# Kernel optimization log

Measured on AMD Instinct MI355X. Metric: run time of the kernel, lower is better.

## Reference

```python
import jax, jax.numpy as jnp
import numpy as np

D_MODEL = 512
NHEAD = 8
HEAD_DIM = D_MODEL // NHEAD


def setup_inputs() -> dict:
    key = jax.random.key(0)
    k1, k2, k3, k4, k5 = jax.random.split(key, 5)
    x = jax.random.normal(k1, (4, 2048, D_MODEL), dtype=jnp.float32)
    s = 1.0 / np.sqrt(D_MODEL)
    W_qkv = jax.random.normal(k2, (D_MODEL, 3 * D_MODEL), dtype=jnp.float32) * s
    b_qkv = jax.random.normal(k3, (3 * D_MODEL,), dtype=jnp.float32) * 0.01
    W_fc = jax.random.normal(k4, (D_MODEL, D_MODEL), dtype=jnp.float32) * s
    b_fc = jax.random.normal(k5, (D_MODEL,), dtype=jnp.float32) * 0.01
    return {"x": x, "W_qkv": W_qkv, "b_qkv": b_qkv, "W_fc": W_fc, "b_fc": b_fc}


def reference(x, W_qkv, b_qkv, W_fc, b_fc):
    b, t, _ = x.shape
    qkv = x @ W_qkv + b_qkv                      # [b, t, 3*d]
    q, k, v = jnp.split(qkv, 3, axis=-1)
    def heads(a):
        return a.reshape(b, t, NHEAD, HEAD_DIM).transpose(0, 2, 1, 3)  # b h t d
    q, k, v = heads(q), heads(k), heads(v)
    scale = HEAD_DIM ** -0.5
    dots = jnp.einsum('bhid,bhjd->bhij', q, k) * scale
    attn = jax.nn.softmax(dots, axis=-1)         # dropout = identity (eval)
    out = jnp.einsum('bhij,bhjd->bhid', attn, v)
    out = out.transpose(0, 2, 1, 3).reshape(b, t, D_MODEL)
    return out @ W_fc + b_fc
```

## Files before the change

kernel.cpp:

```cpp
#include <hip/hip_runtime.h>
#include <hip/hip_bf16.h>
#include <cstddef>
#include <cstdint>

typedef __bf16 bf16_t;
typedef __attribute__((ext_vector_type(8))) __bf16 bf16x8;
typedef __attribute__((ext_vector_type(4))) float f32x4;
typedef __attribute__((ext_vector_type(16))) float f32x16;
typedef __attribute__((ext_vector_type(2))) unsigned uint2v;

#define B_   4
#define T_   2048
#define D_   512
#define H_   8
#define HD_  64
#define BT_  8192
#define N3_  1536

__device__ inline f32x4 mfma16(bf16x8 a, bf16x8 b, f32x4 c) {
  return __builtin_amdgcn_mfma_f32_16x16x32_bf16(a, b, c, 0, 0, 0);
}
__device__ inline f32x16 mfma32(bf16x8 a, bf16x8 b, f32x16 c) {
  return __builtin_amdgcn_mfma_f32_32x32x16_bf16(a, b, c, 0, 0, 0);
}

#define GLOADLDS(lds_base, gsrc)                                           \
  __builtin_amdgcn_global_load_lds(                                        \
      (const __attribute__((address_space(1))) unsigned int*)(gsrc),       \
      (__attribute__((address_space(3))) unsigned int*)(lds_base), 16, 0, 0)


__global__ __launch_bounds__(256) void k_castx(const float* __restrict__ in,
                                               bf16_t* __restrict__ out) {
  const size_t i = ((size_t)blockIdx.x * 256 + threadIdx.x) * 8;
  f32x4 v0 = *reinterpret_cast<const f32x4*>(&in[i]);
  f32x4 v1 = *reinterpret_cast<const f32x4*>(&in[i + 4]);
  bf16x8 o;
#pragma unroll
  for (int k = 0; k < 4; ++k) { o[k] = (bf16_t)v0[k]; o[4 + k] = (bf16_t)v1[k]; }
  *reinterpret_cast<bf16x8*>(&out[i]) = o;
}

__global__ __launch_bounds__(256) void k_tcast(const float* __restrict__ in,
                                               bf16_t* __restrict__ out,
                                               int R, int C) {
  __shared__ bf16_t tile[64][72];
  const int c0 = blockIdx.x * 64, r0 = blockIdx.y * 64;
  const int t = threadIdx.x;
  const int rr = t >> 4;
  const int cc = (t & 15) * 4;
#pragma unroll
  for (int p = 0; p < 4; ++p) {
    int r = p * 16 + rr;
    f32x4 v = *reinterpret_cast<const f32x4*>(&in[(size_t)(r0 + r) * C + c0 + cc]);
#pragma unroll
    for (int i = 0; i < 4; ++i) tile[cc + i][r] = (bf16_t)v[i];
  }
  __syncthreads();
#pragma unroll
  for (int p = 0; p < 4; ++p) {
    int c = p * 16 + rr;
    union { uint2 u; bf16_t e[4]; } pk;
#pragma unroll
    for (int i = 0; i < 4; ++i) pk.e[i] = tile[c][cc + i];
    *reinterpret_cast<uint2*>(&out[(size_t)(c0 + c) * R + r0 + cc]) = pk.u;
  }
}

__global__ __launch_bounds__(512) void k_gemm_qkv(
    const bf16_t* __restrict__ Xb, const bf16_t* __restrict__ Wt,
    const float* __restrict__ bias, bf16_t* __restrict__ Qp,
    bf16_t* __restrict__ Kp, bf16_t* __restrict__ Vp) {
  __shared__ __align__(16) char smem[128 * 136 * 2];
  bf16_t* As = (bf16_t*)smem;
  bf16_t* Bs = (bf16_t*)(smem + 8192);
  const int bm0 = blockIdx.x * 128, bn0 = blockIdx.y * 128;
  const int tid = threadIdx.x, lane = tid & 63, wid = tid >> 6;
  const int wm = wid >> 1, wn = wid & 1;
  const int srow = 16 * wid + (lane >> 2);
  const int scol = (lane & 3) * 8;
  f32x4 acc[2][4] = {};
  for (int kt = 0; kt < D_; kt += 32) {
    GLOADLDS(&As[(16 * wid) * 32], &Xb[(size_t)(bm0 + srow) * D_ + kt + scol]);
    GLOADLDS(&Bs[(16 * wid) * 32], &Wt[(size_t)(bn0 + srow) * D_ + kt + scol]);
    __syncthreads();
    const int fr = lane & 15, kq = (lane >> 4) * 8;
    bf16x8 af[2], bfr[4];
#pragma unroll
    for (int m = 0; m < 2; ++m)
      af[m] = *reinterpret_cast<const bf16x8*>(&As[(wm * 32 + m * 16 + fr) * 32 + kq]);
#pragma unroll
    for (int n = 0; n < 4; ++n)
      bfr[n] = *reinterpret_cast<const bf16x8*>(&Bs[(wn * 64 + n * 16 + fr) * 32 + kq]);
#pragma unroll
    for (int m = 0; m < 2; ++m)
#pragma unroll
      for (int n = 0; n < 4; ++n)
        acc[m][n] = mfma16(af[m], bfr[n], acc[m][n]);
    __syncthreads();
  }
  const float c1 = 0.18033688011112042f;
  const int fr = lane & 15, fq = lane >> 4;
  const int sec = bn0 >> 9;
  const int bb = bm0 >> 11, tt0 = bm0 & 2047;
  const int hb = (bn0 & 511) >> 6;
  bf16_t* Cs = (bf16_t*)smem;
  const int LDC = 136;
  if (sec < 2) {
#pragma unroll
    for (int n = 0; n < 4; ++n) {
      int col = wn * 64 + n * 16 + fr;
      float bv = bias[bn0 + col];
#pragma unroll
      for (int m = 0; m < 2; ++m) {
        int rbase = wm * 32 + m * 16 + fq * 4;
#pragma unroll
        for (int j = 0; j < 4; ++j) {
          float fv = acc[m][n][j] + bv;
          if (sec == 0) fv *= c1;
          Cs[(rbase + j) * LDC + col] = (bf16_t)fv;
        }
      }
    }
  } else {
#pragma unroll
    for (int n = 0; n < 4; ++n) {
      int col = wn * 64 + n * 16 + fr;
      float bv = bias[bn0 + col];
#pragma unroll
      for (int m = 0; m < 2; ++m) {
        int rbase = wm * 32 + m * 16 + fq * 4;
        union { uint2 u; bf16_t e[4]; } pk;
#pragma unroll
        for (int j = 0; j < 4; ++j) pk.e[j] = (bf16_t)(acc[m][n][j] + bv);
        *reinterpret_cast<uint2*>(&Cs[col * LDC + rbase]) = pk.u;
      }
    }
  }
  __syncthreads();
#pragma unroll
  for (int c = 0; c < 4; ++c) {
    const int chunk = wid * 4 + c;
    if (sec < 2) {
      const int h2 = chunk >> 4, rb = (chunk >> 2) & 3, dc = chunk & 3;
      bf16x8 v = *reinterpret_cast<const bf16x8*>(
          &Cs[(rb * 32 + (lane & 31)) * LDC + h2 * 64 + dc * 16 + (lane >> 5) * 8]);
      bf16_t* dst = sec == 0 ? Qp : Kp;
      size_t a = (((size_t)((bb * H_ + hb + h2) * 64 + (tt0 >> 5) + rb)) * 4 + dc) * 512 +
                 lane * 8;
      *reinterpret_cast<bf16x8*>(&dst[a]) = v;
    } else {
      const int h2 = chunk >> 4, tb = (chunk >> 1) & 7, dh = chunk & 1;
      bf16x8 v = *reinterpret_cast<const bf16x8*>(
          &Cs[(h2 * 64 + dh * 32 + (lane & 31)) * LDC + tb * 16 + (lane >> 5) * 8]);
      size_t a = (((size_t)((bb * H_ + hb + h2) * 128 + (tt0 >> 4) + tb)) * 2 + dh) * 512 +
                 lane * 8;
      *reinterpret_cast<bf16x8*>(&Vp[a]) = v;
    }
  }
}

__global__ __launch_bounds__(512) void k_gemm_fc(
    const bf16_t* __restrict__ A, const bf16_t* __restrict__ Wt,
    const float* __restrict__ bias, float* __restrict__ Out) {
  __shared__ __align__(16) bf16_t As[128 * 32];
  __shared__ __align__(16) bf16_t Bs[64 * 32];
  const int bm0 = blockIdx.x * 128, bn0 = blockIdx.y * 64;
  const int tid = threadIdx.x, lane = tid & 63, wid = tid >> 6;
  const int wm = wid >> 2, wn = wid & 3;
  const int wm2 = wid >> 1, wn2 = wid & 1;
  const int srow = 16 * wid + (lane >> 2);
  const int scol = (lane & 3) * 8;
  (void)wm; (void)wn;
  f32x4 acc[2][2] = {};
  for (int kt = 0; kt < D_; kt += 32) {
    GLOADLDS(&As[(16 * wid) * 32], &A[(size_t)(bm0 + srow) * D_ + kt + scol]);
    if (wid < 4)
      GLOADLDS(&Bs[(16 * wid) * 32],
               &Wt[(size_t)(bn0 + 16 * wid + (lane >> 2)) * D_ + kt + scol]);
    __syncthreads();
    const int fr = lane & 15, kq = (lane >> 4) * 8;
    bf16x8 af[2], bfr[2];
#pragma unroll
    for (int m = 0; m < 2; ++m)
      af[m] = *reinterpret_cast<const bf16x8*>(&As[(wm2 * 32 + m * 16 + fr) * 32 + kq]);
#pragma unroll
    for (int n = 0; n < 2; ++n)
      bfr[n] = *reinterpret_cast<const bf16x8*>(&Bs[(wn2 * 32 + n * 16 + fr) * 32 + kq]);
#pragma unroll
    for (int m = 0; m < 2; ++m)
#pragma unroll
      for (int n = 0; n < 2; ++n)
        acc[m][n] = mfma16(af[m], bfr[n], acc[m][n]);
    __syncthreads();
  }
  const int fr = lane & 15, fq = lane >> 4;
#pragma unroll
  for (int n = 0; n < 2; ++n) {
    int ng = bn0 + wn2 * 32 + n * 16 + fr;
    float bv = bias[ng];
#pragma unroll
    for (int m = 0; m < 2; ++m) {
      int mg = bm0 + wm2 * 32 + m * 16 + fq * 4;
#pragma unroll
      for (int j = 0; j < 4; ++j)
        Out[(size_t)(mg + j) * D_ + ng] = acc[m][n][j] + bv;
    }
  }
}

__device__ __forceinline__ void loadKf(const bf16_t* __restrict__ b, int tile,
                                       bf16x8 (&kf)[4]) {
#pragma unroll
  for (int ds = 0; ds < 4; ++ds)
    kf[ds] = *reinterpret_cast<const bf16x8*>(b + ((size_t)(tile * 4 + ds) << 9));
}
__device__ __forceinline__ void loadVf(const bf16_t* __restrict__ b, int c0,
                                       bf16x8 (&v)[4]) {
  v[0] = *reinterpret_cast<const bf16x8*>(b + ((size_t)(c0 * 2 + 0) << 9));
  v[1] = *reinterpret_cast<const bf16x8*>(b + ((size_t)(c0 * 2 + 2) << 9));
  v[2] = *reinterpret_cast<const bf16x8*>(b + ((size_t)(c0 * 2 + 1) << 9));
  v[3] = *reinterpret_cast<const bf16x8*>(b + ((size_t)(c0 * 2 + 3) << 9));
}

__device__ __forceinline__ f32x16 qk32(const bf16x8 (&kf)[4],
                                       const bf16x8 (&qf)[4]) {
  f32x16 s;
#pragma unroll
  for (int i = 0; i < 16; ++i) s[i] = 0.f;
  s = mfma32(kf[0], qf[0], s);
  s = mfma32(kf[1], qf[1], s);
  s = mfma32(kf[2], qf[2], s);
  s = mfma32(kf[3], qf[3], s);
  return s;
}

__device__ __forceinline__ void pv_acc(f32x16& s, const bf16x8 (&v)[4],
                                       f32x16& o0, f32x16& o1, float& lsum) {
  float p[16];
#pragma unroll
  for (int r = 0; r < 16; ++r) p[r] = __builtin_exp2f(s[r]);
  lsum += (((p[0] + p[1]) + (p[2] + p[3])) + ((p[4] + p[5]) + (p[6] + p[7]))) +
          (((p[8] + p[9]) + (p[10] + p[11])) +
           ((p[12] + p[13]) + (p[14] + p[15])));
  union PW { __hip_bfloat162 h; unsigned u; };
#pragma unroll
  for (int ks = 0; ks < 2; ++ks) {
    const int rb = ks * 8;
    PW t0, t1, t2, t3;
    t0.h = __float22bfloat162_rn(make_float2(p[rb + 0], p[rb + 1]));
    t1.h = __float22bfloat162_rn(make_float2(p[rb + 2], p[rb + 3]));
    t2.h = __float22bfloat162_rn(make_float2(p[rb + 4], p[rb + 5]));
    t3.h = __float22bfloat162_rn(make_float2(p[rb + 6], p[rb + 7]));
    uint2v r02 = __builtin_amdgcn_permlane32_swap(t0.u, t2.u, false, false);
    uint2v r13 = __builtin_amdgcn_permlane32_swap(t1.u, t3.u, false, false);
    union { unsigned u[4]; bf16x8 vv; } af;
    af.u[0] = r02[0]; af.u[1] = r13[0]; af.u[2] = r02[1]; af.u[3] = r13[1];
    if (ks == 0) {
      o0 = mfma32(af.vv, v[0], o0);
      o1 = mfma32(af.vv, v[2], o1);
    } else {
      o0 = mfma32(af.vv, v[1], o0);
      o1 = mfma32(af.vv, v[3], o1);
    }
  }
}

__global__ __launch_bounds__(512, 2) void k_attn(
    const bf16_t* __restrict__ Qp, const bf16_t* __restrict__ Kp,
    const bf16_t* __restrict__ Vp, bf16_t* __restrict__ Ctx) {
  __shared__ float Olds[4][32][64];
  __shared__ float Llds[4][64];
  const int lin = blockIdx.x;
  const int logical = (lin & 7) * 64 + (lin >> 3);
  const int bh = logical >> 4, qblk = logical & 15;
  const int tid = threadIdx.x, lane = tid & 63, wid = tid >> 6;
  const int qt = wid & 3, half = wid >> 2;
  const int q0 = qblk * 128 + qt * 32;
  const int tbase = half * 32;
  const bf16_t* Qb = Qp + ((size_t)(bh * 64 + (q0 >> 5)) << 11) + lane * 8;
  const bf16_t* Kb = Kp + ((size_t)bh << 17) + lane * 8;
  const bf16_t* Vb = Vp + ((size_t)bh << 17) + lane * 8;
  bf16x8 qf[4];
#pragma unroll
  for (int ds = 0; ds < 4; ++ds)
    qf[ds] = *reinterpret_cast<const bf16x8*>(Qb + ((size_t)ds << 9));
  f32x16 o0, o1;
#pragma unroll
  for (int i = 0; i < 16; ++i) { o0[i] = 0.f; o1[i] = 0.f; }
  float lsum = 0.f;
  bf16x8 kfA[4], kfB[4], vA[4], vB[4];
  loadKf(Kb, tbase + 0, kfA);
  loadKf(Kb, tbase + 1, kfB);
  loadVf(Vb, (tbase << 1) + 0, vA);
  loadVf(Vb, (tbase << 1) + 2, vB);
  f32x16 sA = qk32(kfA, qf);
  for (int st = 0; st < 32; st += 2) {
    const bool more = (st + 2 < 32);
    f32x16 sB = qk32(kfB, qf);
    if (more) loadKf(Kb, tbase + st + 2, kfA);
    pv_acc(sA, vA, o0, o1, lsum);
    if (more) loadVf(Vb, ((tbase + st) << 1) + 4, vA);
    if (more) sA = qk32(kfA, qf);
    if (more) loadKf(Kb, tbase + st + 3, kfB);
    pv_acc(sB, vB, o0, o1, lsum);
    if (more) loadVf(Vb, ((tbase + st) << 1) + 6, vB);
  }
  lsum += __shfl_xor(lsum, 32);
  if (half == 1) {
#pragma unroll
    for (int r = 0; r < 16; ++r) {
      Olds[qt][r][lane] = o0[r];
      Olds[qt][16 + r][lane] = o1[r];
    }
    Llds[qt][lane] = lsum;
  }
  __syncthreads();
  if (half == 1) return;
  const float lfull = lsum + Llds[qt][lane];
  const float linv = 1.f / lfull;
  const int bb = bh >> 3, hh = bh & 7;
  const int ql = lane & 31;
#pragma unroll
  for (int r = 0; r < 16; ++r) {
    const int qr = (r & 3) + 8 * (r >> 2) + 4 * (lane >> 5);
    const float li = __shfl(linv, qr);
    float v0 = (o0[r] + Olds[qt][r][lane]) * li;
    float v1 = (o1[r] + Olds[qt][16 + r][lane]) * li;
    size_t base = ((size_t)(bb * T_ + q0 + qr)) * D_ + hh * HD_ + ql;
    Ctx[base] = (bf16_t)v0;
    Ctx[base + 32] = (bf16_t)v1;
  }
}

extern "C" void kernel_launch(void* const* d_in, const int* in_sizes, int n_in,
                              void* d_out, int out_size, void* d_ws,
                              size_t ws_size, hipStream_t stream) {
  const float* x    = (const float*)d_in[0];
  const float* Wqkv = (const float*)d_in[1];
  const float* bqkv = (const float*)d_in[2];
  const float* Wfc  = (const float*)d_in[3];
  const float* bfc  = (const float*)d_in[4];
  float* out = (float*)d_out;

  char* ws = (char*)d_ws;
  size_t off = 0;
  bf16_t* Wqt = (bf16_t*)(ws + off); off += (size_t)N3_ * D_ * 2;
  bf16_t* Wft = (bf16_t*)(ws + off); off += (size_t)D_ * D_ * 2;
  bf16_t* Qb  = (bf16_t*)(ws + off); off += (size_t)BT_ * D_ * 2;
  bf16_t* Kb  = (bf16_t*)(ws + off); off += (size_t)BT_ * D_ * 2;
  bf16_t* Vb  = (bf16_t*)(ws + off); off += (size_t)BT_ * D_ * 2;
  bf16_t* Ctx = (bf16_t*)(ws + off); off += (size_t)BT_ * D_ * 2;
  bf16_t* Xb  = Ctx;

  k_castx<<<BT_ * D_ / (256 * 8), 256, 0, stream>>>(x, Xb);
  k_tcast<<<dim3(N3_ / 64, D_ / 64), 256, 0, stream>>>(Wqkv, Wqt, D_, N3_);
  k_tcast<<<dim3(D_ / 64, D_ / 64), 256, 0, stream>>>(Wfc, Wft, D_, D_);
  k_gemm_qkv<<<dim3(BT_ / 128, N3_ / 128), 512, 0, stream>>>(Xb, Wqt, bqkv, Qb,
                                                             Kb, Vb);
  k_attn<<<512, 512, 0, stream>>>(Qb, Kb, Vb, Ctx);
  k_gemm_fc<<<dim3(BT_ / 128, D_ / 64), 512, 0, stream>>>(Ctx, Wft, bfc, out);
}
```

Before: 101.8 us.

## Widen QKV GEMM K-tile to 64 with XOR-swizzled LDS, reuse zero accumulator

The QKV projection GEMM now stages 64-wide K slices per iteration instead of 32, which halves the number of barrier pairs. Each row's 16-byte chunks are XOR-swizzled by row index to avoid LDS bank conflicts on the fragment reads. Separately, the attention QK^T MFMA chain now starts from a pinned zero register vector rather than re-zeroing 16 registers per tile. The cost is more LDS per block and more fragment registers in the GEMM, which may reduce occupancy.

```diff
diff --git a/kernel.cpp b/kernel.cpp
--- a/kernel.cpp
+++ b/kernel.cpp
@@ -71,32 +71,55 @@
     const bf16_t* __restrict__ Xb, const bf16_t* __restrict__ Wt,
     const float* __restrict__ bias, bf16_t* __restrict__ Qp,
     bf16_t* __restrict__ Kp, bf16_t* __restrict__ Vp) {
-  __shared__ __align__(16) char smem[128 * 136 * 2];
+  __shared__ __align__(16) char smem[34816];
   bf16_t* As = (bf16_t*)smem;
-  bf16_t* Bs = (bf16_t*)(smem + 8192);
+  bf16_t* Bs = (bf16_t*)(smem + 16384);
   const int bm0 = blockIdx.x * 128, bn0 = blockIdx.y * 128;
   const int tid = threadIdx.x, lane = tid & 63, wid = tid >> 6;
   const int wm = wid >> 1, wn = wid & 1;
-  const int srow = 16 * wid + (lane >> 2);
-  const int scol = (lane & 3) * 8;
+  const int rl = lane >> 3;
+  const int s8 = lane & 7;
   f32x4 acc[2][4] = {};
-  for (int kt = 0; kt < D_; kt += 32) {
-    GLOADLDS(&As[(16 * wid) * 32], &Xb[(size_t)(bm0 + srow) * D_ + kt + scol]);
-    GLOADLDS(&Bs[(16 * wid) * 32], &Wt[(size_t)(bn0 + srow) * D_ + kt + scol]);
+  for (int kt = 0; kt < D_; kt += 64) {
+#pragma unroll
+    for (int r = 0; r < 2; ++r) {
+      const int row = 16 * wid + 8 * r + rl;
+      const int sl = (s8 ^ (row & 7)) * 8;
+      GLOADLDS(&As[(16 * wid + 8 * r) * 64],
+               &Xb[(size_t)(bm0 + row) * D_ + kt + sl]);
+      GLOADLDS(&Bs[(16 * wid + 8 * r) * 64],
+               &Wt[(size_t)(bn0 + row) * D_ + kt + sl]);
+    }
     __syncthreads();
-    const int fr = lane & 15, kq = (lane >> 4) * 8;
-    bf16x8 af[2], bfr[4];
-#pragma unroll
-    for (int m = 0; m < 2; ++m)
-      af[m] = *reinterpret_cast<const bf16x8*>(&As[(wm * 32 + m * 16 + fr) * 32 + kq]);
-#pragma unroll
-    for (int n = 0; n < 4; ++n)
-      bfr[n] = *reinterpret_cast<const bf16x8*>(&Bs[(wn * 64 + n * 16 + fr) * 32 + kq]);
-#pragma unroll
-    for (int m = 0; m < 2; ++m)
-#pragma unroll
-      for (int n = 0; n < 4; ++n)
-        acc[m][n] = mfma16(af[m], bfr[n], acc[m][n]);
+    const int fr = lane & 15, kq8 = lane >> 4;
+    bf16x8 af[2][2], bfr[4][2];
+#pragma unroll
+    for (int m = 0; m < 2; ++m) {
+      const int row = wm * 32 + m * 16 + fr;
+#pragma unroll
+      for (int kh = 0; kh < 2; ++kh) {
+        const int sL = kh * 4 + kq8;
+        af[m][kh] = *reinterpret_cast<const bf16x8*>(
+            &As[row * 64 + ((sL ^ (row & 7)) * 8)]);
+      }
+    }
+#pragma unroll
+    for (int n = 0; n < 4; ++n) {
+      const int row = wn * 64 + n * 16 + fr;
+#pragma unroll
+      for (int kh = 0; kh < 2; ++kh) {
+        const int sL = kh * 4 + kq8;
+        bfr[n][kh] = *reinterpret_cast<const bf16x8*>(
+            &Bs[row * 64 + ((sL ^ (row & 7)) * 8)]);
+      }
+    }
+#pragma unroll
+    for (int kh = 0; kh < 2; ++kh)
+#pragma unroll
+      for (int m = 0; m < 2; ++m)
+#pragma unroll
+        for (int n = 0; n < 4; ++n)
+          acc[m][n] = mfma16(af[m][kh], bfr[n][kh], acc[m][n]);
     __syncthreads();
   }
   const float c1 = 0.18033688011112042f;
@@ -167,11 +190,9 @@
   __shared__ __align__(16) bf16_t Bs[64 * 32];
   const int bm0 = blockIdx.x * 128, bn0 = blockIdx.y * 64;
   const int tid = threadIdx.x, lane = tid & 63, wid = tid >> 6;
-  const int wm = wid >> 2, wn = wid & 3;
   const int wm2 = wid >> 1, wn2 = wid & 1;
   const int srow = 16 * wid + (lane >> 2);
   const int scol = (lane & 3) * 8;
-  (void)wm; (void)wn;
   f32x4 acc[2][2] = {};
   for (int kt = 0; kt < D_; kt += 32) {
     GLOADLDS(&As[(16 * wid) * 32], &A[(size_t)(bm0 + srow) * D_ + kt + scol]);
@@ -224,11 +245,9 @@
 }
 
 __device__ __forceinline__ f32x16 qk32(const bf16x8 (&kf)[4],
-                                       const bf16x8 (&qf)[4]) {
-  f32x16 s;
-#pragma unroll
-  for (int i = 0; i < 16; ++i) s[i] = 0.f;
-  s = mfma32(kf[0], qf[0], s);
+                                       const bf16x8 (&qf)[4],
+                                       const f32x16& zro) {
+  f32x16 s = mfma32(kf[0], qf[0], zro);
   s = mfma32(kf[1], qf[1], s);
   s = mfma32(kf[2], qf[2], s);
   s = mfma32(kf[3], qf[3], s);
@@ -285,23 +304,24 @@
 #pragma unroll
   for (int ds = 0; ds < 4; ++ds)
     qf[ds] = *reinterpret_cast<const bf16x8*>(Qb + ((size_t)ds << 9));
-  f32x16 o0, o1;
-#pragma unroll
-  for (int i = 0; i < 16; ++i) { o0[i] = 0.f; o1[i] = 0.f; }
+  f32x16 o0, o1, zro;
+#pragma unroll
+  for (int i = 0; i < 16; ++i) { o0[i] = 0.f; o1[i] = 0.f; zro[i] = 0.f; }
+  asm volatile("" : "+v"(zro));
   float lsum = 0.f;
   bf16x8 kfA[4], kfB[4], vA[4], vB[4];
   loadKf(Kb, tbase + 0, kfA);
   loadKf(Kb, tbase + 1, kfB);
   loadVf(Vb, (tbase << 1) + 0, vA);
   loadVf(Vb, (tbase << 1) + 2, vB);
-  f32x16 sA = qk32(kfA, qf);
+  f32x16 sA = qk32(kfA, qf, zro);
   for (int st = 0; st < 32; st += 2) {
     const bool more = (st + 2 < 32);
-    f32x16 sB = qk32(kfB, qf);
+    f32x16 sB = qk32(kfB, qf, zro);
     if (more) loadKf(Kb, tbase + st + 2, kfA);
     pv_acc(sA, vA, o0, o1, lsum);
     if (more) loadVf(Vb, ((tbase + st) << 1) + 4, vA);
-    if (more) sA = qk32(kfA, qf);
+    if (more) sA = qk32(kfA, qf, zro);
     if (more) loadKf(Kb, tbase + st + 3, kfB);
     pv_acc(sB, vB, o0, o1, lsum);
     if (more) loadVf(Vb, ((tbase + st) << 1) + 6, vB);
```

Result: faster. 99.28 us (-2.5%).
